# Kernel optimization log

Hardware: AMD Instinct MI355X
Metric: run time of the kernel (lower is better)

Reference implementation:

```python
import jax, jax.numpy as jnp
import numpy as np

B = 2048
NF = 256          # n_feature
IN = NF + 1       # input dim of embedder
EH = 128          # embedder hidden
E = 64            # embedded_dim
H = 64            # lstm_size (== embedded_dim -> simple attention, no projection)
SH = 256          # policy shared hidden
SD = 128          # shared_dim
NA = NF + 1       # n_action
N_SHUFFLE = 4


def setup_inputs() -> dict:
    key = jax.random.key(0)
    ks = jax.random.split(key, 20)
    s = 0.05
    inp = {
        "state": jax.random.normal(ks[0], (B, NF), jnp.float32),
        "acquired": jax.random.randint(ks[1], (B, NF), 0, 2, jnp.int64),
        # embedder MLP: IN -> EH (relu) -> E
        "W_e1": jax.random.normal(ks[2], (IN, EH), jnp.float32) * s,
        "b_e1": jnp.zeros((EH,), jnp.float32),
        "W_e2": jax.random.normal(ks[3], (EH, E), jnp.float32) * s,
        "b_e2": jnp.zeros((E,), jnp.float32),
        # LSTMCell(E, H), gate order i,f,g,o
        "W_ih": jax.random.normal(ks[4], (E, 4 * H), jnp.float32) * s,
        "W_hh": jax.random.normal(ks[5], (H, 4 * H), jnp.float32) * s,
        "b_ih": jnp.zeros((4 * H,), jnp.float32),
        "b_hh": jnp.zeros((4 * H,), jnp.float32),
        # DuelingNet shared MLP: (H+E) -> SH (relu) -> SD
        "W_s1": jax.random.normal(ks[6], (H + E, SH), jnp.float32) * s,
        "b_s1": jnp.zeros((SH,), jnp.float32),
        "W_s2": jax.random.normal(ks[7], (SH, SD), jnp.float32) * s,
        "b_s2": jnp.zeros((SD,), jnp.float32),
        # pi_net: SD -> SD (relu) -> NA
        "W_p1": jax.random.normal(ks[8], (SD, SD), jnp.float32) * s,
        "b_p1": jnp.zeros((SD,), jnp.float32),
        "W_p2": jax.random.normal(ks[9], (SD, NA), jnp.float32) * s,
        "b_p2": jnp.zeros((NA,), jnp.float32),
        # v_net: SD -> SD (relu) -> 1
        "W_v1": jax.random.normal(ks[10], (SD, SD), jnp.float32) * s,
        "b_v1": jnp.zeros((SD,), jnp.float32),
        "W_v2": jax.random.normal(ks[11], (SD, 1), jnp.float32) * s,
        "b_v2": jnp.zeros((1,), jnp.float32),
    }
    return inp


def reference(state, acquired, W_e1, b_e1, W_e2, b_e2, W_ih, W_hh, b_ih, b_hh,
              W_s1, b_s1, W_s2, b_s2, W_p1, b_p1, W_p2, b_p2, W_v1, b_v1, W_v2, b_v2):
    # ---- state2input: sort acquired one-hot ids descending, gather state values ----
    oh = acquired * (jnp.arange(NF, dtype=acquired.dtype) + 1)          # [B,NF]
    order = jnp.argsort(-oh, axis=-1)                                   # descending, stable
    sorted_oh = jnp.take_along_axis(oh, order, axis=-1)
    onehot = jax.nn.one_hot(sorted_oh, NF + 1, dtype=state.dtype)[:, :, 1:]  # [B,NF,NF]
    vals = jnp.take_along_axis(state, order, axis=-1)[..., None]        # [B,NF,1]
    inputs = jnp.concatenate([vals, onehot], axis=-1)                   # [B,NF,NF+1]
    lengths = jnp.sum(acquired, axis=-1)                                # [B]

    # ---- SetEncoder: per-token embedder MLP ----
    hid = jax.nn.relu(inputs @ W_e1 + b_e1)
    emb = hid @ W_e2 + b_e2                                             # [B,NF,E]

    mask = jnp.arange(NF)[None, :] < lengths[:, None]                   # valid positions
    qt = jnp.zeros((state.shape[0], H), state.dtype)
    ct = qt
    NEG = jnp.asarray(-1e9, state.dtype)
    for _ in range(N_SHUFFLE):
        logits = jnp.einsum('ble,be->bl', emb, qt)
        logits = jnp.where(mask, logits, NEG)
        w = jax.nn.softmax(logits, axis=-1)                             # [B,NF]
        attended = jnp.einsum('bl,ble->be', w, emb)                     # [B,E]
        gates = attended @ W_ih + qt @ W_hh + b_ih + b_hh
        i_g, f_g, g_g, o_g = jnp.split(gates, 4, axis=-1)
        ct = jax.nn.sigmoid(f_g) * ct + jax.nn.sigmoid(i_g) * jnp.tanh(g_g)
        qt = jax.nn.sigmoid(o_g) * jnp.tanh(ct)

    encoded = jnp.concatenate([attended, qt], axis=-1)                  # [B,H+E]
    encoded = jnp.where((lengths > 0)[:, None], encoded, jnp.zeros((), state.dtype))

    # ---- DuelingNet ----
    sh = jax.nn.relu(jax.nn.relu(encoded @ W_s1 + b_s1) @ W_s2 + b_s2)
    adv = jax.nn.relu(sh @ W_p1 + b_p1) @ W_p2 + b_p2                   # [B,NA]
    v = jax.nn.relu(sh @ W_v1 + b_v1) @ W_v2 + b_v2                     # [B,1]
    return v + (adv - jnp.mean(adv, axis=1, keepdims=True))
```

## Files before the change

kernel.cpp:

```cpp
#include <hip/hip_runtime.h>
#include <math.h>

namespace {

constexpr int NF   = 256;
constexpr int NFP  = NF + 16;
constexpr int EH   = 128;
constexpr int E    = 64;
constexpr int H    = 64;
constexpr int SHD  = 256;
constexpr int SD   = 128;
constexpr int NA   = 257;
constexpr int NSHUF = 4;

__device__ __forceinline__ float fsig(float x) {
  return 1.f / (1.f + __expf(-x));
}
__device__ __forceinline__ float ftanh(float x) {
  return 1.f - 2.f / (__expf(2.f * x) + 1.f);
}

__global__ __launch_bounds__(64)
void seqnet(
    const float* __restrict__ state, const int* __restrict__ acquired,
    const float* __restrict__ We1, const float* __restrict__ be1,
    const float* __restrict__ We2, const float* __restrict__ be2,
    const float* __restrict__ Wih, const float* __restrict__ Whh,
    const float* __restrict__ bih, const float* __restrict__ bhh,
    const float* __restrict__ Ws1, const float* __restrict__ bs1,
    const float* __restrict__ Ws2, const float* __restrict__ bs2,
    const float* __restrict__ Wp1, const float* __restrict__ bp1,
    const float* __restrict__ Wp2, const float* __restrict__ bp2,
    const float* __restrict__ Wv1, const float* __restrict__ bv1,
    const float* __restrict__ Wv2, const float* __restrict__ bv2,
    float* __restrict__ out)
{
  const int row = blockIdx.x;
  const int l   = threadIdx.x;
  const int g   = l >> 4;
  const int sub = l & 15;
  const int kbase = sub * 8;

  __shared__ int   id_s[NFP];
  __shared__ __align__(16) float val_s[NFP];
  __shared__ __align__(16) float w_s[NFP];
  __shared__ __align__(16) float rv_s[EH];
  __shared__ __align__(16) float u_s[EH];
  __shared__ __align__(16) float enc_s[EH];
  __shared__ __align__(16) float gates_s[256];
  __shared__ __align__(16) float t1_s[SHD];
  __shared__ __align__(16) float sh_s[SD];
  __shared__ __align__(16) float a1_s[SD];
  __shared__ __align__(16) float v1_s[SD];

  const int* __restrict__ arow = acquired + row * NF;
  #pragma unroll
  for (int j = 0; j < 4; ++j) { id_s[l + 64 * j] = 0; val_s[l + 64 * j] = 0.f; }
  if (l < 16) { id_s[NF + l] = 0; val_s[NF + l] = 0.f; w_s[NF + l] = 0.f; }
  int aiv[4];
  unsigned long long m0, m1, m2, m3;
  aiv[0] = (arow[l]       != 0); m0 = __ballot(aiv[0]);
  aiv[1] = (arow[64 + l]  != 0); m1 = __ballot(aiv[1]);
  aiv[2] = (arow[128 + l] != 0); m2 = __ballot(aiv[2]);
  aiv[3] = (arow[192 + l] != 0); m3 = __ballot(aiv[3]);
  const int pc0 = __popcll(m0), pc1 = __popcll(m1);
  const int pc2 = __popcll(m2), pc3 = __popcll(m3);
  const int L = pc0 + pc1 + pc2 + pc3;
  {
    const int suf1 = pc1 + pc2 + pc3, suf2 = pc2 + pc3, suf3 = pc3;
    if (aiv[0]) { const int r = (int)__popcll((m0 >> l) >> 1) + suf1;
      id_s[r] = l + 1;       val_s[r] = state[row * NF + l]; }
    if (aiv[1]) { const int r = (int)__popcll((m1 >> l) >> 1) + suf2;
      id_s[r] = 64 + l + 1;  val_s[r] = state[row * NF + 64 + l]; }
    if (aiv[2]) { const int r = (int)__popcll((m2 >> l) >> 1) + suf3;
      id_s[r] = 128 + l + 1; val_s[r] = state[row * NF + 128 + l]; }
    if (aiv[3]) { const int r = (int)__popcll((m3 >> l) >> 1);
      id_s[r] = 192 + l + 1; val_s[r] = state[row * NF + 192 + l]; }
  }

  float ct_r = 0.f;

  const float4 z0 = *(const float4*)(We1 + kbase);
  const float4 z1 = *(const float4*)(We1 + kbase + 4);
  const float4 c0 = *(const float4*)(be1 + kbase);
  const float4 c1 = *(const float4*)(be1 + kbase + 4);

  if (L > 0) {
    const float invL = 1.f / (float)L;
    const int ntok  = (L > g) ? ((L - g + 3) >> 2) : 0;
    const int nquad = (ntok + 3) >> 2;
    for (int it = 0; it < NSHUF; ++it) {
      if (it == 0) {
        #pragma unroll
        for (int j = 0; j < 4; ++j) w_s[l + 64 * j] = (l + 64 * j < L) ? invL : 0.f;
      } else {
        {
          const float4* __restrict__ r0 = (const float4*)(We2 + l * E);
          const float4* __restrict__ r1 = (const float4*)(We2 + (64 + l) * E);
          float a0 = 0.f, a1 = 0.f, b0 = 0.f, b1 = 0.f;
          #pragma unroll
          for (int j = 0; j < 16; j += 2) {
            const float4 x0 = r0[j], x1 = r1[j];
            const float4 q4 = *(const float4*)(enc_s + 64 + 4 * j);
            a0 = fmaf(x0.x, q4.x, a0); a1 = fmaf(x1.x, q4.x, a1);
            a0 = fmaf(x0.y, q4.y, a0); a1 = fmaf(x1.y, q4.y, a1);
            a0 = fmaf(x0.z, q4.z, a0); a1 = fmaf(x1.z, q4.z, a1);
            a0 = fmaf(x0.w, q4.w, a0); a1 = fmaf(x1.w, q4.w, a1);
            const float4 y0 = r0[j + 1], y1 = r1[j + 1];
            const float4 q5 = *(const float4*)(enc_s + 64 + 4 * j + 4);
            b0 = fmaf(y0.x, q5.x, b0); b1 = fmaf(y1.x, q5.x, b1);
            b0 = fmaf(y0.y, q5.y, b0); b1 = fmaf(y1.y, q5.y, b1);
            b0 = fmaf(y0.z, q5.z, b0); b1 = fmaf(y1.z, q5.z, b1);
            b0 = fmaf(y0.w, q5.w, b0); b1 = fmaf(y1.w, q5.w, b1);
          }
          rv_s[l] = a0 + b0; rv_s[64 + l] = a1 + b1;
        }
        const float4 ra = *(const float4*)(rv_s + kbase);
        const float4 rb = *(const float4*)(rv_s + kbase + 4);
        float vcur[4]; float4 gA[4], gB[4];
        #pragma unroll
        for (int s = 0; s < 4; ++s) {
          const int tk = g + 4 * s;
          const int idt = id_s[tk]; vcur[s] = val_s[tk];
          gA[s] = *(const float4*)(We1 + idt * EH + kbase);
          gB[s] = *(const float4*)(We1 + idt * EH + kbase + 4);
        }
        for (int j = 0; j < nquad; ++j) {
          const int bnext = 16 * (j + 1) + g;
          float vnxt[4]; float4 gA2[4], gB2[4];
          #pragma unroll
          for (int s = 0; s < 4; ++s) {
            const int tk = bnext + 4 * s;
            const int idt = id_s[tk]; vnxt[s] = val_s[tk];
            gA2[s] = *(const float4*)(We1 + idt * EH + kbase);
            gB2[s] = *(const float4*)(We1 + idt * EH + kbase + 4);
          }
          float p[4];
          #pragma unroll
          for (int s = 0; s < 4; ++s) {
            float h, pp;
            h = fmaxf(fmaf(vcur[s], z0.x, gA[s].x) + c0.x, 0.f); pp = h * ra.x;
            h = fmaxf(fmaf(vcur[s], z0.y, gA[s].y) + c0.y, 0.f); pp = fmaf(h, ra.y, pp);
            h = fmaxf(fmaf(vcur[s], z0.z, gA[s].z) + c0.z, 0.f); pp = fmaf(h, ra.z, pp);
            h = fmaxf(fmaf(vcur[s], z0.w, gA[s].w) + c0.w, 0.f); pp = fmaf(h, ra.w, pp);
            h = fmaxf(fmaf(vcur[s], z1.x, gB[s].x) + c1.x, 0.f); pp = fmaf(h, rb.x, pp);
            h = fmaxf(fmaf(vcur[s], z1.y, gB[s].y) + c1.y, 0.f); pp = fmaf(h, rb.y, pp);
            h = fmaxf(fmaf(vcur[s], z1.z, gB[s].z) + c1.z, 0.f); pp = fmaf(h, rb.z, pp);
            h = fmaxf(fmaf(vcur[s], z1.w, gB[s].w) + c1.w, 0.f); pp = fmaf(h, rb.w, pp);
            p[s] = pp;
          }
          #pragma unroll
          for (int s = 0; s < 4; ++s) {
            p[s] += __shfl_xor(p[s], 1); p[s] += __shfl_xor(p[s], 2);
            p[s] += __shfl_xor(p[s], 4); p[s] += __shfl_xor(p[s], 8);
          }
          if (sub == 0) {
            const int bcur = 16 * j + g;
            w_s[bcur]      = p[0]; w_s[bcur + 4]  = p[1];
            w_s[bcur + 8]  = p[2]; w_s[bcur + 12] = p[3];
          }
          #pragma unroll
          for (int s = 0; s < 4; ++s) { vcur[s] = vnxt[s]; gA[s] = gA2[s]; gB[s] = gB2[s]; }
        }
        float x0 = (l < L)       ? w_s[l]       : -1e30f;
        float x1 = (64 + l < L)  ? w_s[64 + l]  : -1e30f;
        float x2 = (128 + l < L) ? w_s[128 + l] : -1e30f;
        float x3 = (192 + l < L) ? w_s[192 + l] : -1e30f;
        float mx = fmaxf(fmaxf(x0, x1), fmaxf(x2, x3));
        #pragma unroll
        for (int d = 32; d > 0; d >>= 1) mx = fmaxf(mx, __shfl_xor(mx, d));
        const float e0 = (l < L)       ? __expf(x0 - mx) : 0.f;
        const float e1 = (64 + l < L)  ? __expf(x1 - mx) : 0.f;
        const float e2 = (128 + l < L) ? __expf(x2 - mx) : 0.f;
        const float e3 = (192 + l < L) ? __expf(x3 - mx) : 0.f;
        float s = (e0 + e1) + (e2 + e3);
        #pragma unroll
        for (int d = 32; d > 0; d >>= 1) s += __shfl_xor(s, d);
        const float inv = 1.f / s;
        w_s[l]       = e0 * inv;
        w_s[64 + l]  = e1 * inv;
        w_s[128 + l] = e2 * inv;
        w_s[192 + l] = e3 * inv;
      }

      float4 ua{0, 0, 0, 0}, ub{0, 0, 0, 0};
      {
        float vcur[4], wcur[4]; float4 gA[4], gB[4];
        #pragma unroll
        for (int s = 0; s < 4; ++s) {
          const int tk = g + 4 * s;
          const int idt = id_s[tk]; vcur[s] = val_s[tk]; wcur[s] = w_s[tk];
          gA[s] = *(const float4*)(We1 + idt * EH + kbase);
          gB[s] = *(const float4*)(We1 + idt * EH + kbase + 4);
        }
        for (int j = 0; j < nquad; ++j) {
          const int bnext = 16 * (j + 1) + g;
          float vnxt[4], wnxt[4]; float4 gA2[4], gB2[4];
          #pragma unroll
          for (int s = 0; s < 4; ++s) {
            const int tk = bnext + 4 * s;
            const int idt = id_s[tk]; vnxt[s] = val_s[tk]; wnxt[s] = w_s[tk];
            gA2[s] = *(const float4*)(We1 + idt * EH + kbase);
            gB2[s] = *(const float4*)(We1 + idt * EH + kbase + 4);
          }
          #pragma unroll
          for (int s = 0; s < 4; ++s) {
            const float vt = vcur[s], wt = wcur[s];
            float h;
            h = fmaxf(fmaf(vt, z0.x, gA[s].x) + c0.x, 0.f); ua.x = fmaf(wt, h, ua.x);
            h = fmaxf(fmaf(vt, z0.y, gA[s].y) + c0.y, 0.f); ua.y = fmaf(wt, h, ua.y);
            h = fmaxf(fmaf(vt, z0.z, gA[s].z) + c0.z, 0.f); ua.z = fmaf(wt, h, ua.z);
            h = fmaxf(fmaf(vt, z0.w, gA[s].w) + c0.w, 0.f); ua.w = fmaf(wt, h, ua.w);
            h = fmaxf(fmaf(vt, z1.x, gB[s].x) + c1.x, 0.f); ub.x = fmaf(wt, h, ub.x);
            h = fmaxf(fmaf(vt, z1.y, gB[s].y) + c1.y, 0.f); ub.y = fmaf(wt, h, ub.y);
            h = fmaxf(fmaf(vt, z1.z, gB[s].z) + c1.z, 0.f); ub.z = fmaf(wt, h, ub.z);
            h = fmaxf(fmaf(vt, z1.w, gB[s].w) + c1.w, 0.f); ub.w = fmaf(wt, h, ub.w);
          }
          #pragma unroll
          for (int s = 0; s < 4; ++s) {
            vcur[s] = vnxt[s]; wcur[s] = wnxt[s]; gA[s] = gA2[s]; gB[s] = gB2[s];
          }
        }
      }
      #pragma unroll
      for (int d = 16; d <= 32; d <<= 1) {
        ua.x += __shfl_xor(ua.x, d); ua.y += __shfl_xor(ua.y, d);
        ua.z += __shfl_xor(ua.z, d); ua.w += __shfl_xor(ua.w, d);
        ub.x += __shfl_xor(ub.x, d); ub.y += __shfl_xor(ub.y, d);
        ub.z += __shfl_xor(ub.z, d); ub.w += __shfl_xor(ub.w, d);
      }
      if (l < 16) {
        *(float4*)(u_s + l * 8)     = ua;
        *(float4*)(u_s + l * 8 + 4) = ub;
      }

      {
        float a0 = 0.f, a1 = 0.f, a2 = 0.f, a3 = 0.f;
        #pragma unroll 4
        for (int k = 0; k < EH; k += 4) {
          a0 = fmaf(u_s[k],     We2[(k)     * E + l], a0);
          a1 = fmaf(u_s[k + 1], We2[(k + 1) * E + l], a1);
          a2 = fmaf(u_s[k + 2], We2[(k + 2) * E + l], a2);
          a3 = fmaf(u_s[k + 3], We2[(k + 3) * E + l], a3);
        }
        enc_s[l] = (a0 + a1) + (a2 + a3) + be2[l];
      }

      {
        float4 acc0{0, 0, 0, 0}, acc1{0, 0, 0, 0};
        #pragma unroll 2
        for (int e = 0; e < E; e += 2) {
          const float av0 = enc_s[e], av1 = enc_s[e + 1];
          const float4 w0 = *(const float4*)(Wih + (e)     * 256 + 4 * l);
          const float4 w1 = *(const float4*)(Wih + (e + 1) * 256 + 4 * l);
          acc0.x = fmaf(av0, w0.x, acc0.x); acc0.y = fmaf(av0, w0.y, acc0.y);
          acc0.z = fmaf(av0, w0.z, acc0.z); acc0.w = fmaf(av0, w0.w, acc0.w);
          acc1.x = fmaf(av1, w1.x, acc1.x); acc1.y = fmaf(av1, w1.y, acc1.y);
          acc1.z = fmaf(av1, w1.z, acc1.z); acc1.w = fmaf(av1, w1.w, acc1.w);
        }
        if (it > 0) {
          #pragma unroll 2
          for (int e = 0; e < E; e += 2) {
            const float qv0 = enc_s[64 + e], qv1 = enc_s[64 + e + 1];
            const float4 w0 = *(const float4*)(Whh + (e)     * 256 + 4 * l);
            const float4 w1 = *(const float4*)(Whh + (e + 1) * 256 + 4 * l);
            acc0.x = fmaf(qv0, w0.x, acc0.x); acc0.y = fmaf(qv0, w0.y, acc0.y);
            acc0.z = fmaf(qv0, w0.z, acc0.z); acc0.w = fmaf(qv0, w0.w, acc0.w);
            acc1.x = fmaf(qv1, w1.x, acc1.x); acc1.y = fmaf(qv1, w1.y, acc1.y);
            acc1.z = fmaf(qv1, w1.z, acc1.z); acc1.w = fmaf(qv1, w1.w, acc1.w);
          }
        }
        const float4 bi = *(const float4*)(bih + 4 * l);
        const float4 bh = *(const float4*)(bhh + 4 * l);
        float4 gacc;
        gacc.x = acc0.x + acc1.x + bi.x + bh.x;
        gacc.y = acc0.y + acc1.y + bi.y + bh.y;
        gacc.z = acc0.z + acc1.z + bi.z + bh.z;
        gacc.w = acc0.w + acc1.w + bi.w + bh.w;
        *(float4*)(gates_s + 4 * l) = gacc;
        const float gi = gates_s[l];
        const float gf = gates_s[64 + l];
        const float gg = gates_s[128 + l];
        const float go = gates_s[192 + l];
        ct_r = fsig(gf) * ct_r + fsig(gi) * ftanh(gg);
        enc_s[64 + l] = fsig(go) * ftanh(ct_r);
      }
    }
  } else {
    enc_s[l] = 0.f; enc_s[64 + l] = 0.f;
  }

  {
    float4 acc0{0, 0, 0, 0}, acc1{0, 0, 0, 0};
    #pragma unroll 2
    for (int k = 0; k < EH; k += 2) {
      const float e0 = enc_s[k], e1 = enc_s[k + 1];
      const float4 w0 = *(const float4*)(Ws1 + (k)     * SHD + 4 * l);
      const float4 w1 = *(const float4*)(Ws1 + (k + 1) * SHD + 4 * l);
      acc0.x = fmaf(e0, w0.x, acc0.x); acc0.y = fmaf(e0, w0.y, acc0.y);
      acc0.z = fmaf(e0, w0.z, acc0.z); acc0.w = fmaf(e0, w0.w, acc0.w);
      acc1.x = fmaf(e1, w1.x, acc1.x); acc1.y = fmaf(e1, w1.y, acc1.y);
      acc1.z = fmaf(e1, w1.z, acc1.z); acc1.w = fmaf(e1, w1.w, acc1.w);
    }
    const float4 b4 = *(const float4*)(bs1 + 4 * l);
    t1_s[4 * l]     = fmaxf(acc0.x + acc1.x + b4.x, 0.f);
    t1_s[4 * l + 1] = fmaxf(acc0.y + acc1.y + b4.y, 0.f);
    t1_s[4 * l + 2] = fmaxf(acc0.z + acc1.z + b4.z, 0.f);
    t1_s[4 * l + 3] = fmaxf(acc0.w + acc1.w + b4.w, 0.f);
  }
  {
    float2 acc0{0, 0}, acc1{0, 0};
    #pragma unroll 2
    for (int k = 0; k < SHD; k += 2) {
      const float t0 = t1_s[k], t1v = t1_s[k + 1];
      const float2 w0 = *(const float2*)(Ws2 + (k)     * SD + 2 * l);
      const float2 w1 = *(const float2*)(Ws2 + (k + 1) * SD + 2 * l);
      acc0.x = fmaf(t0, w0.x, acc0.x); acc0.y = fmaf(t0, w0.y, acc0.y);
      acc1.x = fmaf(t1v, w1.x, acc1.x); acc1.y = fmaf(t1v, w1.y, acc1.y);
    }
    sh_s[2 * l]     = fmaxf(acc0.x + acc1.x + bs2[2 * l],     0.f);
    sh_s[2 * l + 1] = fmaxf(acc0.y + acc1.y + bs2[2 * l + 1], 0.f);
  }
  {
    float2 pa{0, 0}, qa{0, 0};
    #pragma unroll 2
    for (int k = 0; k < SD; ++k) {
      const float sv = sh_s[k];
      const float2 wp = *(const float2*)(Wp1 + k * SD + 2 * l);
      const float2 wv = *(const float2*)(Wv1 + k * SD + 2 * l);
      pa.x = fmaf(sv, wp.x, pa.x); pa.y = fmaf(sv, wp.y, pa.y);
      qa.x = fmaf(sv, wv.x, qa.x); qa.y = fmaf(sv, wv.y, qa.y);
    }
    a1_s[2 * l]     = fmaxf(pa.x + bp1[2 * l],     0.f);
    a1_s[2 * l + 1] = fmaxf(pa.y + bp1[2 * l + 1], 0.f);
    v1_s[2 * l]     = fmaxf(qa.x + bv1[2 * l],     0.f);
    v1_s[2 * l + 1] = fmaxf(qa.y + bv1[2 * l + 1], 0.f);
  }
  float a0 = 0.f, a1 = 0.f, a2 = 0.f, a3 = 0.f;
  #pragma unroll 2
  for (int k = 0; k < SD; ++k) {
    const float av = a1_s[k];
    const float* __restrict__ wr = Wp2 + k * NA;
    a0 = fmaf(av, wr[l],       a0);
    a1 = fmaf(av, wr[64 + l],  a1);
    a2 = fmaf(av, wr[128 + l], a2);
    a3 = fmaf(av, wr[192 + l], a3);
  }
  a0 += bp2[l]; a1 += bp2[64 + l]; a2 += bp2[128 + l]; a3 += bp2[192 + l];
  float c4 = fmaf(a1_s[2 * l], Wp2[(2 * l) * NA + 256],
                  a1_s[2 * l + 1] * Wp2[(2 * l + 1) * NA + 256]);
  #pragma unroll
  for (int d = 32; d > 0; d >>= 1) c4 += __shfl_xor(c4, d);
  const float adv4 = c4 + bp2[256];
  float vv = fmaf(v1_s[l], Wv2[l], v1_s[64 + l] * Wv2[64 + l]);
  #pragma unroll
  for (int d = 32; d > 0; d >>= 1) vv += __shfl_xor(vv, d);
  const float v = vv + bv2[0];
  float ss = (a0 + a1) + (a2 + a3);
  #pragma unroll
  for (int d = 32; d > 0; d >>= 1) ss += __shfl_xor(ss, d);
  const float mean = (ss + adv4) * (1.f / (float)NA);

  const float base = v - mean;
  float* __restrict__ orow = out + row * NA;
  orow[l]       = base + a0;
  orow[64 + l]  = base + a1;
  orow[128 + l] = base + a2;
  orow[192 + l] = base + a3;
  if (l == 0) orow[256] = base + adv4;
}

}

extern "C" void kernel_launch(void* const* d_in, const int* in_sizes, int n_in,
                              void* d_out, int out_size, void* d_ws, size_t ws_size,
                              hipStream_t stream) {
  const float* state    = (const float*)d_in[0];
  const int*   acquired = (const int*)d_in[1];
  const float* We1 = (const float*)d_in[2];
  const float* be1 = (const float*)d_in[3];
  const float* We2 = (const float*)d_in[4];
  const float* be2 = (const float*)d_in[5];
  const float* Wih = (const float*)d_in[6];
  const float* Whh = (const float*)d_in[7];
  const float* bih = (const float*)d_in[8];
  const float* bhh = (const float*)d_in[9];
  const float* Ws1 = (const float*)d_in[10];
  const float* bs1 = (const float*)d_in[11];
  const float* Ws2 = (const float*)d_in[12];
  const float* bs2 = (const float*)d_in[13];
  const float* Wp1 = (const float*)d_in[14];
  const float* bp1 = (const float*)d_in[15];
  const float* Wp2 = (const float*)d_in[16];
  const float* bp2 = (const float*)d_in[17];
  const float* Wv1 = (const float*)d_in[18];
  const float* bv1 = (const float*)d_in[19];
  const float* Wv2 = (const float*)d_in[20];
  const float* bv2 = (const float*)d_in[21];
  float* out = (float*)d_out;

  const int Bn = in_sizes[0] / NF;
  hipLaunchKernelGGL(seqnet, dim3(Bn), dim3(64), 0, stream,
                     state, acquired, We1, be1, We2, be2, Wih, Whh, bih, bhh,
                     Ws1, bs1, Ws2, bs2, Wp1, bp1, Wp2, bp2, Wv1, bv1, Wv2, bv2,
                     out);
}
```

Baseline: 142.3 us.

## Pre-transpose Wp2/We2 for vectorized dot products and deepen gather prefetch

Adds a small pre-kernel that transposes Wp2 and We2 into a workspace, so the per-row kernel can run float4 contiguous dot products against shared-memory vectors instead of strided scalar loads. It also splits the We1 gather pipeline so index and value loads from LDS run two blocks ahead and the global row loads one block ahead, hiding LDS latency behind the address computation. The cost is an extra kernel launch per call and larger shared padding (NFP is 32 entries past NF), plus more live registers in the prefetch loops.

Result: slower. 183.2 us (+28.7%).

```diff
diff --git a/kernel.cpp b/kernel.cpp
--- a/kernel.cpp
+++ b/kernel.cpp
@@ -4,7 +4,7 @@
 namespace {
 
 constexpr int NF   = 256;
-constexpr int NFP  = NF + 16;
+constexpr int NFP  = NF + 32;
 constexpr int EH   = 128;
 constexpr int E    = 64;
 constexpr int H    = 64;
@@ -18,6 +18,21 @@
 }
 __device__ __forceinline__ float ftanh(float x) {
   return 1.f - 2.f / (__expf(2.f * x) + 1.f);
+}
+
+__global__ __launch_bounds__(256) void transpose_wk(
+    const float* __restrict__ Wp2, const float* __restrict__ We2,
+    float* __restrict__ Wp2T, float* __restrict__ We2T)
+{
+  const int tid = blockIdx.x * 256 + threadIdx.x;
+  if (tid < NA * SD) {
+    const int c = tid / SD, k = tid - c * SD;
+    Wp2T[tid] = Wp2[k * NA + c];
+  } else if (tid < NA * SD + E * EH) {
+    const int t2 = tid - NA * SD;
+    const int c = t2 / EH, k = t2 - c * EH;
+    We2T[t2] = We2[k * E + c];
+  }
 }
 
 __global__ __launch_bounds__(64)
@@ -30,9 +45,10 @@
     const float* __restrict__ Ws1, const float* __restrict__ bs1,
     const float* __restrict__ Ws2, const float* __restrict__ bs2,
     const float* __restrict__ Wp1, const float* __restrict__ bp1,
-    const float* __restrict__ Wp2, const float* __restrict__ bp2,
+    const float* __restrict__ Wp2T, const float* __restrict__ bp2,
     const float* __restrict__ Wv1, const float* __restrict__ bv1,
     const float* __restrict__ Wv2, const float* __restrict__ bv2,
+    const float* __restrict__ We2T,
     float* __restrict__ out)
 {
   const int row = blockIdx.x;
@@ -56,7 +72,7 @@
   const int* __restrict__ arow = acquired + row * NF;
   #pragma unroll
   for (int j = 0; j < 4; ++j) { id_s[l + 64 * j] = 0; val_s[l + 64 * j] = 0.f; }
-  if (l < 16) { id_s[NF + l] = 0; val_s[NF + l] = 0.f; w_s[NF + l] = 0.f; }
+  if (l < 32) { id_s[NF + l] = 0; val_s[NF + l] = 0.f; w_s[NF + l] = 0.f; }
   int aiv[4];
   unsigned long long m0, m1, m2, m3;
   aiv[0] = (arow[l]       != 0); m0 = __ballot(aiv[0]);
@@ -117,23 +133,29 @@
         }
         const float4 ra = *(const float4*)(rv_s + kbase);
         const float4 rb = *(const float4*)(rv_s + kbase + 4);
-        float vcur[4]; float4 gA[4], gB[4];
+        int idp[4]; float vcur[4], vnx[4];
         #pragma unroll
         for (int s = 0; s < 4; ++s) {
-          const int tk = g + 4 * s;
-          const int idt = id_s[tk]; vcur[s] = val_s[tk];
-          gA[s] = *(const float4*)(We1 + idt * EH + kbase);
-          gB[s] = *(const float4*)(We1 + idt * EH + kbase + 4);
+          vcur[s] = val_s[g + 4 * s];
+          idp[s]  = id_s[16 + g + 4 * s]; vnx[s] = val_s[16 + g + 4 * s];
+        }
+        float4 gA[4], gB[4];
+        #pragma unroll
+        for (int s = 0; s < 4; ++s) {
+          const int id0 = id_s[g + 4 * s];
+          gA[s] = *(const float4*)(We1 + id0 * EH + kbase);
+          gB[s] = *(const float4*)(We1 + id0 * EH + kbase + 4);
         }
         for (int j = 0; j < nquad; ++j) {
-          const int bnext = 16 * (j + 1) + g;
-          float vnxt[4]; float4 gA2[4], gB2[4];
-          #pragma unroll
-          for (int s = 0; s < 4; ++s) {
-            const int tk = bnext + 4 * s;
-            const int idt = id_s[tk]; vnxt[s] = val_s[tk];
-            gA2[s] = *(const float4*)(We1 + idt * EH + kbase);
-            gB2[s] = *(const float4*)(We1 + idt * EH + kbase + 4);
+          const int b2 = 16 * (j + 2) + g;
+          int idn[4]; float vn[4];
+          #pragma unroll
+          for (int s = 0; s < 4; ++s) { idn[s] = id_s[b2 + 4 * s]; vn[s] = val_s[b2 + 4 * s]; }
+          float4 gA2[4], gB2[4];
+          #pragma unroll
+          for (int s = 0; s < 4; ++s) {
+            gA2[s] = *(const float4*)(We1 + idp[s] * EH + kbase);
+            gB2[s] = *(const float4*)(We1 + idp[s] * EH + kbase + 4);
           }
           float p[4];
           #pragma unroll
@@ -160,7 +182,10 @@
             w_s[bcur + 8]  = p[2]; w_s[bcur + 12] = p[3];
           }
           #pragma unroll
-          for (int s = 0; s < 4; ++s) { vcur[s] = vnxt[s]; gA[s] = gA2[s]; gB[s] = gB2[s]; }
+          for (int s = 0; s < 4; ++s) {
+            vcur[s] = vnx[s]; vnx[s] = vn[s]; idp[s] = idn[s];
+            gA[s] = gA2[s]; gB[s] = gB2[s];
+          }
         }
         float x0 = (l < L)       ? w_s[l]       : -1e30f;
         float x1 = (64 + l < L)  ? w_s[64 + l]  : -1e30f;
@@ -185,23 +210,32 @@
 
       float4 ua{0, 0, 0, 0}, ub{0, 0, 0, 0};
       {
-        float vcur[4], wcur[4]; float4 gA[4], gB[4];
+        int idp[4]; float vcur[4], wcur[4], vnx[4], wnx[4];
         #pragma unroll
         for (int s = 0; s < 4; ++s) {
-          const int tk = g + 4 * s;
-          const int idt = id_s[tk]; vcur[s] = val_s[tk]; wcur[s] = w_s[tk];
-          gA[s] = *(const float4*)(We1 + idt * EH + kbase);
-          gB[s] = *(const float4*)(We1 + idt * EH + kbase + 4);
+          vcur[s] = val_s[g + 4 * s]; wcur[s] = w_s[g + 4 * s];
+          idp[s]  = id_s[16 + g + 4 * s];
+          vnx[s]  = val_s[16 + g + 4 * s]; wnx[s] = w_s[16 + g + 4 * s];
+        }
+        float4 gA[4], gB[4];
+        #pragma unroll
+        for (int s = 0; s < 4; ++s) {
+          const int id0 = id_s[g + 4 * s];
+          gA[s] = *(const float4*)(We1 + id0 * EH + kbase);
+          gB[s] = *(const float4*)(We1 + id0 * EH + kbase + 4);
         }
         for (int j = 0; j < nquad; ++j) {
-          const int bnext = 16 * (j + 1) + g;
-          float vnxt[4], wnxt[4]; float4 gA2[4], gB2[4];
-          #pragma unroll
-          for (int s = 0; s < 4; ++s) {
-            const int tk = bnext + 4 * s;
-            const int idt = id_s[tk]; vnxt[s] = val_s[tk]; wnxt[s] = w_s[tk];
-            gA2[s] = *(const float4*)(We1 + idt * EH + kbase);
-            gB2[s] = *(const float4*)(We1 + idt * EH + kbase + 4);
+          const int b2 = 16 * (j + 2) + g;
+          int idn[4]; float vn[4], wn[4];
+          #pragma unroll
+          for (int s = 0; s < 4; ++s) {
+            idn[s] = id_s[b2 + 4 * s]; vn[s] = val_s[b2 + 4 * s]; wn[s] = w_s[b2 + 4 * s];
+          }
+          float4 gA2[4], gB2[4];
+          #pragma unroll
+          for (int s = 0; s < 4; ++s) {
+            gA2[s] = *(const float4*)(We1 + idp[s] * EH + kbase);
+            gB2[s] = *(const float4*)(We1 + idp[s] * EH + kbase + 4);
           }
           #pragma unroll
           for (int s = 0; s < 4; ++s) {
@@ -218,7 +252,9 @@
           }
           #pragma unroll
           for (int s = 0; s < 4; ++s) {
-            vcur[s] = vnxt[s]; wcur[s] = wnxt[s]; gA[s] = gA2[s]; gB[s] = gB2[s];
+            vcur[s] = vnx[s]; wcur[s] = wnx[s];
+            vnx[s] = vn[s];   wnx[s] = wn[s];   idp[s] = idn[s];
+            gA[s] = gA2[s];   gB[s] = gB2[s];
           }
         }
       }
@@ -235,13 +271,15 @@
       }
 
       {
+        const float4* __restrict__ wt = (const float4*)(We2T + l * EH);
+        const float4* __restrict__ uv = (const float4*)u_s;
         float a0 = 0.f, a1 = 0.f, a2 = 0.f, a3 = 0.f;
-        #pragma unroll 4
-        for (int k = 0; k < EH; k += 4) {
-          a0 = fmaf(u_s[k],     We2[(k)     * E + l], a0);
-          a1 = fmaf(u_s[k + 1], We2[(k + 1) * E + l], a1);
-          a2 = fmaf(u_s[k + 2], We2[(k + 2) * E + l], a2);
-          a3 = fmaf(u_s[k + 3], We2[(k + 3) * E + l], a3);
+        #pragma unroll 8
+        for (int kk = 0; kk < 32; ++kk) {
+          const float4 w = wt[kk];
+          const float4 u = uv[kk];
+          a0 = fmaf(u.x, w.x, a0); a1 = fmaf(u.y, w.y, a1);
+          a2 = fmaf(u.z, w.z, a2); a3 = fmaf(u.w, w.w, a3);
         }
         enc_s[l] = (a0 + a1) + (a2 + a3) + be2[l];
       }
@@ -336,19 +374,30 @@
     v1_s[2 * l]     = fmaxf(qa.x + bv1[2 * l],     0.f);
     v1_s[2 * l + 1] = fmaxf(qa.y + bv1[2 * l + 1], 0.f);
   }
-  float a0 = 0.f, a1 = 0.f, a2 = 0.f, a3 = 0.f;
-  #pragma unroll 2
-  for (int k = 0; k < SD; ++k) {
-    const float av = a1_s[k];
-    const float* __restrict__ wr = Wp2 + k * NA;
-    a0 = fmaf(av, wr[l],       a0);
-    a1 = fmaf(av, wr[64 + l],  a1);
-    a2 = fmaf(av, wr[128 + l], a2);
-    a3 = fmaf(av, wr[192 + l], a3);
-  }
-  a0 += bp2[l]; a1 += bp2[64 + l]; a2 += bp2[128 + l]; a3 += bp2[192 + l];
-  float c4 = fmaf(a1_s[2 * l], Wp2[(2 * l) * NA + 256],
-                  a1_s[2 * l + 1] * Wp2[(2 * l + 1) * NA + 256]);
+  float a0, a1, a2, a3;
+  {
+    float acc[4];
+    const float4* __restrict__ av = (const float4*)a1_s;
+    #pragma unroll
+    for (int jj = 0; jj < 4; ++jj) {
+      const float4* __restrict__ wr = (const float4*)(Wp2T + (l + 64 * jj) * SD);
+      float b0 = 0.f, b1 = 0.f, b2 = 0.f, b3 = 0.f;
+      #pragma unroll 8
+      for (int kk = 0; kk < 32; ++kk) {
+        const float4 w = wr[kk];
+        const float4 a = av[kk];
+        b0 = fmaf(a.x, w.x, b0); b1 = fmaf(a.y, w.y, b1);
+        b2 = fmaf(a.z, w.z, b2); b3 = fmaf(a.w, w.w, b3);
+      }
+      acc[jj] = (b0 + b1) + (b2 + b3);
+    }
+    a0 = acc[0] + bp2[l];
+    a1 = acc[1] + bp2[64 + l];
+    a2 = acc[2] + bp2[128 + l];
+    a3 = acc[3] + bp2[192 + l];
+  }
+  const float2 wc = *(const float2*)(Wp2T + 256 * SD + 2 * l);
+  float c4 = fmaf(a1_s[2 * l], wc.x, a1_s[2 * l + 1] * wc.y);
   #pragma unroll
   for (int d = 32; d > 0; d >>= 1) c4 += __shfl_xor(c4, d);
   const float adv4 = c4 + bp2[256];
@@ -399,9 +448,16 @@
   const float* bv2 = (const float*)d_in[21];
   float* out = (float*)d_out;
 
+  float* Wp2T = (float*)d_ws;
+  float* We2T = Wp2T + NA * SD;
+
+  const int nT = NA * SD + E * EH;
+  hipLaunchKernelGGL(transpose_wk, dim3((nT + 255) / 256), dim3(256), 0, stream,
+                     Wp2, We2, Wp2T, We2T);
+
   const int Bn = in_sizes[0] / NF;
   hipLaunchKernelGGL(seqnet, dim3(Bn), dim3(64), 0, stream,
                      state, acquired, We1, be1, We2, be2, Wih, Whh, bih, bhh,
-                     Ws1, bs1, Ws2, bs2, Wp1, bp1, Wp2, bp2, Wv1, bv1, Wv2, bv2,
-                     out);
-}
+                     Ws1, bs1, Ws2, bs2, Wp1, bp1, Wp2T, bp2, Wv1, bv1, Wv2, bv2,
+                     We2T, out);
+}
```
